# Optimization experiments

Measured on AMD Instinct MI355X. Metric: run time of the kernel, lower is better.

Reference implementation:

```python
import jax, jax.numpy as jnp
import numpy as np

PI = float(np.pi)


def _layernorm(x, g, b, eps=1e-5):
    mu = jnp.mean(x, axis=-1, keepdims=True)
    var = jnp.var(x, axis=-1, keepdims=True)
    return (x - mu) * jax.lax.rsqrt(var + eps) * g + b


def setup_inputs() -> dict:
    key = jax.random.key(0)
    B, L, D, P = 4, 2048, 256, 32
    ks = jax.random.split(key, 16)

    def lin_w(k, fi, fo):
        return (jax.random.normal(k, (fi, fo), dtype=jnp.float32) / np.sqrt(fi)).astype(jnp.float32)

    inp = {
        'x': jax.random.normal(ks[0], (B, L, D), dtype=jnp.float32),
        'pos_phases': jax.random.normal(ks[1], (L, P), dtype=jnp.float32) * PI,
        'w_mem1v': lin_w(ks[2], D, P), 'b_mem1v': jnp.zeros((P,), jnp.float32),
        'w_mem1o': lin_w(ks[3], P, D), 'b_mem1o': jnp.zeros((D,), jnp.float32),
        'w_off': lin_w(ks[4], D + P, P), 'b_off': jnp.zeros((P,), jnp.float32),
        'w_key': lin_w(ks[5], D, P), 'b_key': jnp.zeros((P,), jnp.float32),
        'w_val': lin_w(ks[6], D, D), 'b_val': jnp.zeros((D,), jnp.float32),
        'w_sk1': lin_w(ks[7], 2 * D, D), 'b_sk1': jnp.zeros((D,), jnp.float32),
        'w_sk2': lin_w(ks[8], D, P), 'b_sk2': jnp.zeros((P,), jnp.float32),
        'w_gate': lin_w(ks[9], D, 1), 'b_gate': jnp.zeros((1,), jnp.float32),
        'ln_g': jnp.ones((D,), jnp.float32), 'ln_b': jnp.zeros((D,), jnp.float32),
        'w_out': lin_w(ks[10], D, D), 'b_out': jnp.zeros((D,), jnp.float32),
    }
    return inp


def reference(x, pos_phases, w_mem1v, b_mem1v, w_mem1o, b_mem1o, w_off, b_off,
              w_key, b_key, w_val, b_val, w_sk1, b_sk1, w_sk2, b_sk2,
              w_gate, b_gate, ln_g, ln_b, w_out, b_out):
    B, L, D = x.shape
    P = pos_phases.shape[-1]

    pos_cos = jnp.cos(pos_phases)  # [L,P]
    pos_sin = jnp.sin(pos_phases)

    # Memory 1: flat [B,L,P] phasor cumulative memory
    v1 = x @ w_mem1v + b_mem1v                       # [B,L,P]
    mem1_cos = jnp.cumsum(pos_cos[None] * v1, axis=1)
    mem1_sin = jnp.cumsum(pos_sin[None] * v1, axis=1)

    offset_input = jnp.concatenate([x, jnp.broadcast_to(pos_phases[None], (B, L, P))], axis=-1)
    offset = jnp.tanh(offset_input @ w_off + b_off) * PI
    oc, os = jnp.cos(offset), jnp.sin(offset)
    query_cos = pos_cos[None] * oc - pos_sin[None] * os
    query_sin = pos_sin[None] * oc + pos_cos[None] * os
    pos_ret = (mem1_cos * query_cos + mem1_sin * query_sin) / np.sqrt(P)
    pos_out = pos_ret @ w_mem1o + b_mem1o            # [B,L,D]

    # Memory 2: full [B,L,P,D] phasor KV cumulative memory
    key_phases = jnp.tanh(x @ w_key + b_key) * PI    # [B,L,P]
    key_cos, key_sin = jnp.cos(key_phases), jnp.sin(key_phases)
    values = x @ w_val + b_val                       # [B,L,D]
    store_gate = jax.nn.sigmoid(x @ w_gate + b_gate) # [B,L,1]

    positions = jnp.arange(1, L + 1, dtype=x.dtype)[None, :, None]
    context_avg = jnp.cumsum(x, axis=1) / positions
    h = jax.nn.gelu(jnp.concatenate([x, context_avg], axis=-1) @ w_sk1 + b_sk1, approximate=False)
    storage_phases = jnp.tanh(h @ w_sk2 + b_sk2) * PI  # [B,L,P]

    gated_v = values * store_gate                    # [B,L,D]
    kv_mem_cos = jnp.cumsum(jnp.cos(storage_phases)[..., None] * gated_v[:, :, None, :], axis=1)  # [B,L,P,D]
    kv_mem_sin = jnp.cumsum(jnp.sin(storage_phases)[..., None] * gated_v[:, :, None, :], axis=1)

    gate_cumsum = jnp.clip(jnp.cumsum(store_gate, axis=1), 1.0, None)  # [B,L,1]
    kv_retrieved = jnp.einsum('blpd,blp->bld', kv_mem_cos, key_cos) + \
                   jnp.einsum('blpd,blp->bld', kv_mem_sin, key_sin)
    kv_retrieved = kv_retrieved / (jnp.sqrt(gate_cumsum) * np.sqrt(P))

    combined = pos_out + kv_retrieved
    return x + _layernorm(combined, ln_g, ln_b) @ w_out + b_out
```

## Files before the change

kernel.cpp:

```cpp
#include <hip/hip_runtime.h>
#include <hip/hip_bf16.h>

constexpr int B_ = 4;
constexpr int L_ = 2048;
constexpr int D_ = 256;
constexpr int P_ = 32;
constexpr int CL = 32;
constexpr int NC = L_ / CL;

#define PI_F 3.14159265358979323846f
#define INV_SQRT_P 0.17677669529663687f

typedef __attribute__((ext_vector_type(8))) short short8_t;
typedef __attribute__((ext_vector_type(4))) float floatx4;

static __device__ inline short f2bf(float f) {
  unsigned int u;
  __builtin_memcpy(&u, &f, 4);
  unsigned int r = (u + 0x7fffu + ((u >> 16) & 1u)) >> 16;
  return (short)r;
}
static __device__ inline float bf2f(short s) {
  unsigned int u = ((unsigned int)(unsigned short)s) << 16;
  float f;
  __builtin_memcpy(&f, &u, 4);
  return f;
}

__global__ void wprep(const float* __restrict__ x, const float* __restrict__ pos,
                      const float* __restrict__ w_val, const float* __restrict__ w_mem1v,
                      const float* __restrict__ w_off, const float* __restrict__ b_off,
                      const float* __restrict__ w_key, const float* __restrict__ w_gate,
                      const float* __restrict__ w_sk1, const float* __restrict__ w_out,
                      const float* __restrict__ w_sk2, const float* __restrict__ w_mem1o,
                      short* __restrict__ WA, short* __restrict__ W1,
                      short* __restrict__ WO, short* __restrict__ W2T,
                      short* __restrict__ W1OT,
                      short* __restrict__ xbf, float* __restrict__ poff,
                      float* __restrict__ ctxsum) {
  __shared__ float2 psum[2][128];
  int blk = blockIdx.x, tid = threadIdx.x;
  if (blk < 384) {
    int idx = blk * 256 + tid;
    int n = idx >> 8, k = idx & 255;
    float v;
    if (n < 256) v = w_val[k * 256 + n];
    else if (n < 288) v = w_mem1v[k * 32 + (n - 256)];
    else if (n < 320) v = w_off[k * 32 + (n - 288)];
    else if (n < 352) v = w_key[k * 32 + (n - 320)];
    else if (n == 352) v = w_gate[k];
    else v = 0.f;
    WA[idx] = f2bf(v);
  } else if (blk < 896) {
    int idx = (blk - 384) * 256 + tid;
    int n = idx >> 9, k = idx & 511;
    W1[idx] = f2bf(w_sk1[k * 256 + n]);
  } else if (blk < 1152) {
    int idx = (blk - 896) * 256 + tid;
    int n = idx >> 8, k = idx & 255;
    WO[idx] = f2bf(w_out[k * 256 + n]);
  } else if (blk < 1184) {
    int idx = (blk - 1152) * 256 + tid;
    int p = idx >> 8, k = idx & 255;
    W2T[idx] = f2bf(w_sk2[k * 32 + p]);
  } else if (blk < 1216) {
    int idx = (blk - 1184) * 256 + tid;
    int d = idx >> 5, p = idx & 31;
    W1OT[idx] = f2bf(w_mem1o[p * 256 + d]);
  } else if (blk < 1472) {
    int idx = (blk - 1216) * 256 + tid;
    int l = idx >> 5, p = idx & 31;
    float a = b_off[p];
#pragma unroll 8
    for (int j = 0; j < 32; ++j) a += pos[l * 32 + j] * w_off[(256 + j) * 32 + p];
    poff[idx] = a;
  } else {
    int c2 = blk - 1472;
    int b = c2 >> 6, ch = c2 & 63;
    int d2 = (tid & 127) * 2, h = tid >> 7;
    int tokb = b * L_ + ch * 32 + h * 16;
    float2 xv[16];
#pragma unroll
    for (int i = 0; i < 16; ++i)
      xv[i] = *(const float2*)&x[(tokb + i) * 256 + d2];
    float2 s = {0.f, 0.f};
#pragma unroll
    for (int i = 0; i < 16; ++i) { s.x += xv[i].x; s.y += xv[i].y; }
#pragma unroll
    for (int i = 0; i < 16; ++i) {
      short2 o;
      o.x = f2bf(xv[i].x);
      o.y = f2bf(xv[i].y);
      *(short2*)&xbf[(tokb + i) * 256 + d2] = o;
    }
    psum[h][tid & 127] = s;
    __syncthreads();
    if (h == 0) {
      float2 o = psum[1][tid & 127];
      float2 tot = {s.x + o.x, s.y + o.y};
      *(float2*)&ctxsum[c2 * 256 + d2] = tot;
    }
  }
}

__global__ __launch_bounds__(768, 6) void gemmA3(const short* __restrict__ xbf,
                                                 const short* __restrict__ WA,
                                                 const float* __restrict__ pos,
                                                 const float* __restrict__ poff,
                                                 const float* __restrict__ b_mem1v,
                                                 const float* __restrict__ b_key,
                                                 const float* __restrict__ b_gate,
                                                 const float* __restrict__ b_val,
                                                 float* __restrict__ m1cT,
                                                 float* __restrict__ m1sT,
                                                 float* __restrict__ qc,
                                                 float* __restrict__ qs,
                                                 short* __restrict__ K2bf,
                                                 short* __restrict__ gvT,
                                                 float* __restrict__ sg) {
  __shared__ float YL[16][132];
  __shared__ float gsh[16];
  int tid = threadIdx.x;
  int lane = tid & 63, w = tid >> 6;
  int ml = lane & 15, quad = lane >> 4, kq = quad * 8;
  int bc = blockIdx.x;
  int bc32 = bc >> 1, half = bc & 1;
  int tok0 = bc * 16;
  floatx4 acc[2] = {};
  const short* A0p = &xbf[(tok0 + ml) * 256 + kq];
  const short* Bp = &WA[(w * 32 + ml) * 256 + kq];
#pragma unroll
  for (int ks = 0; ks < 8; ++ks) {
    short8_t a0 = *(const short8_t*)(A0p + ks * 32);
#pragma unroll
    for (int nt = 0; nt < 2; ++nt) {
      short8_t b = *(const short8_t*)(Bp + nt * 16 * 256 + ks * 32);
      acc[nt] = __builtin_amdgcn_mfma_f32_16x16x32_bf16(a0, b, acc[nt], 0, 0, 0);
    }
  }
  if (w >= 8) {
#pragma unroll
    for (int nt = 0; nt < 2; ++nt) {
      int col = (w - 8) * 32 + nt * 16 + ml;
#pragma unroll
      for (int r = 0; r < 4; ++r)
        YL[quad * 4 + r][col] = acc[nt][r];
    }
  }
  __syncthreads();
  if (tid < 512) {
    int t = tid >> 5, p = tid & 31;
    int tok = tok0 + t, l = tok & (L_ - 1);
    int b = tok >> 11;
    float v1 = YL[t][p] + b_mem1v[p];
    float ph = pos[l * 32 + p];
    float pc = cosf(ph), ps = sinf(ph);
    int idxT = (b * 32 + p) * L_ + l;
    m1cT[idxT] = pc * v1;
    m1sT[idxT] = ps * v1;
    float off = tanhf(YL[t][32 + p] + poff[l * 32 + p]) * PI_F;
    float oc = cosf(off), os = sinf(off);
    int gidx = tok * 32 + p;
    qc[gidx] = pc * oc - ps * os;
    qs[gidx] = ps * oc + pc * os;
    float kp = tanhf(YL[t][64 + p] + b_key[p]) * PI_F;
    K2bf[tok * 64 + p] = f2bf(cosf(kp));
    K2bf[tok * 64 + 32 + p] = f2bf(sinf(kp));
    if (p == 0) {
      float g = 1.f / (1.f + expf(-(YL[t][96] + b_gate[0])));
      sg[tok] = g;
      gsh[t] = g;
    }
  }
  __syncthreads();
  if (w < 8) {
#pragma unroll
    for (int nt = 0; nt < 2; ++nt) {
      int d = w * 32 + nt * 16 + ml;
      float bv = b_val[d];
      int t0 = quad * 4;
      short4 o;
      o.x = f2bf((acc[nt][0] + bv) * gsh[t0 + 0]);
      o.y = f2bf((acc[nt][1] + bv) * gsh[t0 + 1]);
      o.z = f2bf((acc[nt][2] + bv) * gsh[t0 + 2]);
      o.w = f2bf((acc[nt][3] + bv) * gsh[t0 + 3]);
      *(short4*)&gvT[(bc32 * 256 + d) * 32 + half * 16 + t0] = o;
    }
  }
}

__global__ void scan_all(float* __restrict__ m1cT, float* __restrict__ m1sT,
                         float* __restrict__ sg, float* __restrict__ ctxsum) {
  int blk = blockIdx.x;
  int tid = threadIdx.x;
  if (blk >= 260) {
    int b = blk - 260;
    int base = b * 64 * 256 + tid;
    float v[64];
#pragma unroll
    for (int c = 0; c < 64; ++c) v[c] = ctxsum[base + c * 256];
    float run = 0.f;
#pragma unroll
    for (int c = 0; c < 64; ++c) {
      ctxsum[base + c * 256] = run;
      run += v[c];
    }
    return;
  }
  __shared__ float wsum[4];
  int lane = tid & 63, w = tid >> 6;
  float* arr;
  int base;
  if (blk < 256) {
    arr = (blk < 128) ? m1cT : m1sT;
    base = (blk & 127) * L_;
  } else {
    arr = sg;
    base = (blk - 256) * L_;
  }
  int sbase = base + w * 512;
  float v[8];
#pragma unroll
  for (int i = 0; i < 8; ++i) v[i] = arr[sbase + i * 64 + lane];
  float carry = 0.f;
#pragma unroll
  for (int i = 0; i < 8; ++i) {
    float vv = v[i];
#pragma unroll
    for (int off = 1; off < 64; off <<= 1) {
      float n = __shfl_up(vv, off, 64);
      if (lane >= off) vv += n;
    }
    vv += carry;
    v[i] = vv;
    carry = __shfl(vv, 63, 64);
  }
  if (lane == 0) wsum[w] = carry;
  __syncthreads();
  float off = 0.f;
  for (int ww = 0; ww < w; ++ww) off += wsum[ww];
#pragma unroll
  for (int i = 0; i < 8; ++i) arr[sbase + i * 64 + lane] = v[i] + off;
}

union __align__(16) CDMem {
  short As[32][520];
  struct { short HS[32][280]; short SPL[64][40]; } h;
};
__global__ __launch_bounds__(1024, 4) void gemmCD(const short* __restrict__ xbf,
                                                  const float* __restrict__ x,
                                                  const float* __restrict__ ctxsum,
                                                  const short* __restrict__ W1,
                                                  const float* __restrict__ b_sk1,
                                                  const short* __restrict__ W2T,
                                                  const float* __restrict__ b_sk2,
                                                  const short* __restrict__ gvT,
                                                  short* __restrict__ SPbf,
                                                  short* __restrict__ UT) {
  __shared__ CDMem sm;
  __shared__ float stmp[4][256];
  int tid = threadIdx.x;
  int bc = blockIdx.x;
  int tok0 = bc * 32;
  int bI = bc >> 6, ch = bc & 63;
  int lane = tid & 63, w = tid >> 6;
  int ml = lane & 15, quad = lane >> 4, kq = quad * 8;
  {
    int row = tid >> 5, c8 = tid & 31;
    *(short8_t*)&sm.As[row][c8 * 8] =
        *(const short8_t*)&xbf[(tok0 + row) * 256 + c8 * 8];
  }
  {
    int d = tid & 255, qh = tid >> 8;
    float cp = ctxsum[(bI * 64 + ch) * 256 + d];
    float xv[8];
    int xb = (tok0 + qh * 8) * 256 + d;
#pragma unroll
    for (int i = 0; i < 8; ++i) xv[i] = x[xb + i * 256];
    float p = 0.f;
#pragma unroll
    for (int i = 0; i < 8; ++i) p += xv[i];
    stmp[qh][d] = p;
    __syncthreads();
    float run = cp;
    for (int j = 0; j < qh; ++j) run += stmp[j][d];
    int l0 = ch * 32 + qh * 8;
#pragma unroll
    for (int i = 0; i < 8; ++i) {
      run += xv[i];
      sm.As[qh * 8 + i][256 + d] = f2bf(run / (float)(l0 + i + 1));
    }
  }
  __syncthreads();
  int n0w = w * 16;
  floatx4 acc[2] = {};
#pragma unroll
  for (int kt = 0; kt < 16; ++kt) {
    short8_t a0 = *(short8_t*)&sm.As[ml][kt * 32 + kq];
    short8_t a1 = *(short8_t*)&sm.As[16 + ml][kt * 32 + kq];
    short8_t b0 = *(const short8_t*)&W1[(n0w + ml) * 512 + kt * 32 + kq];
    acc[0] = __builtin_amdgcn_mfma_f32_16x16x32_bf16(a0, b0, acc[0], 0, 0, 0);
    acc[1] = __builtin_amdgcn_mfma_f32_16x16x32_bf16(a1, b0, acc[1], 0, 0, 0);
  }
  short hv[2][4];
  {
    float bv = b_sk1[n0w + ml];
#pragma unroll
    for (int mt = 0; mt < 2; ++mt)
#pragma unroll
      for (int r = 0; r < 4; ++r) {
        float v = acc[mt][r] + bv;
        float g = 0.5f * v * (1.f + erff(v * 0.70710678118654752f));
        hv[mt][r] = f2bf(g);
      }
  }
  __syncthreads();
#pragma unroll
  for (int mt = 0; mt < 2; ++mt)
#pragma unroll
    for (int r = 0; r < 4; ++r)
      sm.h.HS[mt * 16 + quad * 4 + r][n0w + ml] = hv[mt][r];
  __syncthreads();
  if (w < 4) {
    int th = w & 1, ph = w >> 1;
    floatx4 pacc = {};
#pragma unroll
    for (int s = 0; s < 8; ++s) {
      short8_t a = *(short8_t*)&sm.h.HS[th * 16 + ml][s * 32 + kq];
      short8_t b0 = *(const short8_t*)&W2T[(ph * 16 + ml) * 256 + s * 32 + kq];
      pacc = __builtin_amdgcn_mfma_f32_16x16x32_bf16(a, b0, pacc, 0, 0, 0);
    }
    int p = ph * 16 + ml;
    float bs = b_sk2[p];
#pragma unroll
    for (int r = 0; r < 4; ++r) {
      int tl = th * 16 + quad * 4 + r;
      int tok = tok0 + tl;
      float sp = tanhf(pacc[r] + bs) * PI_F;
      short c = f2bf(cosf(sp)), s2 = f2bf(sinf(sp));
      sm.h.SPL[p][tl] = c;
      sm.h.SPL[32 + p][tl] = s2;
      SPbf[tok * 64 + p] = c;
      SPbf[tok * 64 + 32 + p] = s2;
    }
  }
  __syncthreads();
  short8_t a[4];
#pragma unroll
  for (int mt = 0; mt < 4; ++mt) a[mt] = *(short8_t*)&sm.h.SPL[mt * 16 + ml][kq];
  floatx4 acc3[4] = {};
  {
    int d = w * 16 + ml;
    short8_t b = *(const short8_t*)&gvT[(bc * 256 + d) * 32 + kq];
#pragma unroll
    for (int mt = 0; mt < 4; ++mt)
      acc3[mt] = __builtin_amdgcn_mfma_f32_16x16x32_bf16(a[mt], b, acc3[mt], 0, 0, 0);
  }
#pragma unroll
  for (int mt = 0; mt < 4; ++mt) {
    int d = w * 16 + ml;
    short4 o;
    o.x = f2bf(acc3[mt][0]);
    o.y = f2bf(acc3[mt][1]);
    o.z = f2bf(acc3[mt][2]);
    o.w = f2bf(acc3[mt][3]);
    *(short4*)&UT[(bc * 256 + d) * 64 + mt * 16 + quad * 4] = o;
  }
}

__global__ void kernelE(short* __restrict__ UT) {
  int t = blockIdx.x * 256 + threadIdx.x;
  int pi = t >> 2, j = t & 3;
  int q = pi & 63;
  int d = (pi >> 6) & 255;
  int b = pi >> 14;
  const int cs = 256 * 64;
  int base = ((b * NC) * 256 + d) * 64 + q + j * 16 * cs;
  short v[16];
#pragma unroll
  for (int c = 0; c < 16; ++c) v[c] = UT[base + c * cs];
  float tot = 0.f;
#pragma unroll
  for (int c = 0; c < 16; ++c) tot += bf2f(v[c]);
  int lane = threadIdx.x & 63;
  int gb = lane & ~3;
  float t0 = __shfl(tot, gb + 0, 64);
  float t1 = __shfl(tot, gb + 1, 64);
  float t2 = __shfl(tot, gb + 2, 64);
  float run = (j > 0 ? t0 : 0.f) + (j > 1 ? t1 : 0.f) + (j > 2 ? t2 : 0.f);
#pragma unroll
  for (int c = 0; c < 16; ++c) {
    UT[base + c * cs] = f2bf(run);
    run += bf2f(v[c]);
  }
}

struct __align__(16) FGMem {
  short SL[32][40];
  short PR[32][40];
  float CMB[32][260];
  short CBN[32][280];
  float LG[256], LB[256];
  float scl[32], mu_s[32], rs_s[32];
};
__global__ __launch_bounds__(1024, 4) void fgOut(const short* __restrict__ UT,
                                                 const short* __restrict__ SPbf,
                                                 const short* __restrict__ K2bf,
                                                 const short* __restrict__ gvT,
                                                 const float* __restrict__ sgc,
                                                 const float* __restrict__ m1cT,
                                                 const float* __restrict__ m1sT,
                                                 const float* __restrict__ qc,
                                                 const float* __restrict__ qs,
                                                 const short* __restrict__ W1OT,
                                                 const float* __restrict__ b_mem1o,
                                                 const float* __restrict__ ln_g,
                                                 const float* __restrict__ ln_b,
                                                 const short* __restrict__ WO,
                                                 const float* __restrict__ b_out,
                                                 const float* __restrict__ x,
                                                 float* __restrict__ out) {
  __shared__ FGMem sm;
  int tid5 = threadIdx.x;
  int bc = blockIdx.x;
  int lbase = bc * CL;
  int bb = bc >> 6, lloc = (bc & 63) * 32;
  int lane = tid5 & 63, w = tid5 >> 6;
  int ml = lane & 15, quad = lane >> 4, kq = quad * 8;
  int d0 = w * 16;
  if (tid5 < 32) sm.scl[tid5] = rsqrtf(fmaxf(sgc[lbase + tid5], 1.f)) * INV_SQRT_P;
  if (tid5 >= 256 && tid5 < 512) {
    int d = tid5 - 256;
    sm.LG[d] = ln_g[d];
    sm.LB[d] = ln_b[d];
  }
  short8_t ka0 = *(const short8_t*)&K2bf[(lbase + ml) * 64 + kq];
  short8_t ka1 = *(const short8_t*)&K2bf[(lbase + 16 + ml) * 64 + kq];
  short8_t kb0 = *(const short8_t*)&K2bf[(lbase + ml) * 64 + 32 + kq];
  short8_t kb1 = *(const short8_t*)&K2bf[(lbase + 16 + ml) * 64 + 32 + kq];
  if (w == 0) {
    floatx4 sacc[2][2] = {};
#pragma unroll
    for (int ks2 = 0; ks2 < 2; ++ks2) {
      short8_t a0 = (ks2 == 0) ? ka0 : kb0;
      short8_t a1 = (ks2 == 0) ? ka1 : kb1;
      short8_t b0 = *(const short8_t*)&SPbf[(lbase + ml) * 64 + ks2 * 32 + kq];
      short8_t b1 = *(const short8_t*)&SPbf[(lbase + 16 + ml) * 64 + ks2 * 32 + kq];
      sacc[0][0] = __builtin_amdgcn_mfma_f32_16x16x32_bf16(a0, b0, sacc[0][0], 0, 0, 0);
      sacc[0][1] = __builtin_amdgcn_mfma_f32_16x16x32_bf16(a0, b1, sacc[0][1], 0, 0, 0);
      sacc[1][0] = __builtin_amdgcn_mfma_f32_16x16x32_bf16(a1, b0, sacc[1][0], 0, 0, 0);
      sacc[1][1] = __builtin_amdgcn_mfma_f32_16x16x32_bf16(a1, b1, sacc[1][1], 0, 0, 0);
    }
#pragma unroll
    for (int mt = 0; mt < 2; ++mt)
#pragma unroll
      for (int nt = 0; nt < 2; ++nt)
#pragma unroll
        for (int r = 0; r < 4; ++r) {
          int trow = mt * 16 + quad * 4 + r;
          int scol = nt * 16 + ml;
          float v = (scol <= trow) ? sacc[mt][nt][r] : 0.f;
          sm.SL[trow][scol] = f2bf(v);
        }
  } else {
    int t7 = tid5 - 64;
    for (int i = t7; i < 1024; i += 960) {
      int pp = i >> 5, t = i & 31;
      int gT = (bb * 32 + pp) * L_ + lloc + t;
      int g = (lbase + t) * 32 + pp;
      sm.PR[t][pp] = f2bf((m1cT[gT] * qc[g] + m1sT[gT] * qs[g]) * INV_SQRT_P);
    }
  }
  __syncthreads();
  floatx4 acc[2] = {};
  {
    short8_t b0 = *(const short8_t*)&UT[(bc * 256 + d0 + ml) * 64 + kq];
    short8_t b1 = *(const short8_t*)&UT[(bc * 256 + d0 + ml) * 64 + 32 + kq];
    acc[0] = __builtin_amdgcn_mfma_f32_16x16x32_bf16(ka0, b0, acc[0], 0, 0, 0);
    acc[1] = __builtin_amdgcn_mfma_f32_16x16x32_bf16(ka1, b0, acc[1], 0, 0, 0);
    acc[0] = __builtin_amdgcn_mfma_f32_16x16x32_bf16(kb0, b1, acc[0], 0, 0, 0);
    acc[1] = __builtin_amdgcn_mfma_f32_16x16x32_bf16(kb1, b1, acc[1], 0, 0, 0);
  }
  {
    short8_t a0 = *(short8_t*)&sm.SL[ml][kq];
    short8_t a1 = *(short8_t*)&sm.SL[16 + ml][kq];
    short8_t b = *(const short8_t*)&gvT[(bc * 256 + d0 + ml) * 32 + kq];
    acc[0] = __builtin_amdgcn_mfma_f32_16x16x32_bf16(a0, b, acc[0], 0, 0, 0);
    acc[1] = __builtin_amdgcn_mfma_f32_16x16x32_bf16(a1, b, acc[1], 0, 0, 0);
  }
  floatx4 macc[2] = {};
  {
    short8_t a0 = *(short8_t*)&sm.PR[ml][kq];
    short8_t a1 = *(short8_t*)&sm.PR[16 + ml][kq];
    short8_t b = *(const short8_t*)&W1OT[(d0 + ml) * 32 + kq];
    macc[0] = __builtin_amdgcn_mfma_f32_16x16x32_bf16(a0, b, macc[0], 0, 0, 0);
    macc[1] = __builtin_amdgcn_mfma_f32_16x16x32_bf16(a1, b, macc[1], 0, 0, 0);
  }
  {
    int d = d0 + ml;
    float bm = b_mem1o[d];
#pragma unroll
    for (int mt = 0; mt < 2; ++mt)
#pragma unroll
      for (int r = 0; r < 4; ++r) {
        int t = mt * 16 + quad * 4 + r;
        sm.CMB[t][d] = acc[mt][r] * sm.scl[t] + macc[mt][r] + bm;
      }
  }
  __syncthreads();
  {
    int t = tid5 >> 5, g = tid5 & 31;
    float s = 0.f, s2 = 0.f;
#pragma unroll
    for (int j = 0; j < 8; ++j) {
      float v = sm.CMB[t][g + j * 32];
      s += v;
      s2 += v * v;
    }
#pragma unroll
    for (int m = 1; m < 32; m <<= 1) {
      s += __shfl_xor(s, m, 64);
      s2 += __shfl_xor(s2, m, 64);
    }
    if (g == 0) {
      float mu = s / (float)D_;
      float var = s2 / (float)D_ - mu * mu;
      sm.mu_s[t] = mu;
      sm.rs_s[t] = rsqrtf(var + 1e-5f);
    }
  }
  __syncthreads();
#pragma unroll
  for (int it = 0; it < 8; ++it) {
    int i = it * 1024 + tid5;
    int t = i >> 8, d = i & 255;
    sm.CBN[t][d] = f2bf((sm.CMB[t][d] - sm.mu_s[t]) * sm.rs_s[t] * sm.LG[d] + sm.LB[d]);
  }
  __syncthreads();
  floatx4 acc2[2] = {};
#pragma unroll
  for (int kt = 0; kt < 8; ++kt) {
    short8_t a0 = *(short8_t*)&sm.CBN[ml][kt * 32 + kq];
    short8_t a1 = *(short8_t*)&sm.CBN[16 + ml][kt * 32 + kq];
    short8_t b = *(const short8_t*)&WO[(d0 + ml) * 256 + kt * 32 + kq];
    acc2[0] = __builtin_amdgcn_mfma_f32_16x16x32_bf16(a0, b, acc2[0], 0, 0, 0);
    acc2[1] = __builtin_amdgcn_mfma_f32_16x16x32_bf16(a1, b, acc2[1], 0, 0, 0);
  }
  {
    int n = d0 + ml;
    float bv = b_out[n];
#pragma unroll
    for (int mt = 0; mt < 2; ++mt)
#pragma unroll
      for (int r = 0; r < 4; ++r) {
        int tok = lbase + mt * 16 + quad * 4 + r;
        out[tok * 256 + n] = x[tok * 256 + n] + acc2[mt][r] + bv;
      }
  }
}

extern "C" void kernel_launch(void* const* d_in, const int* in_sizes, int n_in,
                              void* d_out, int out_size, void* d_ws, size_t ws_size,
                              hipStream_t stream) {
  const float* x = (const float*)d_in[0];
  const float* pos = (const float*)d_in[1];
  const float* w_mem1v = (const float*)d_in[2];
  const float* b_mem1v = (const float*)d_in[3];
  const float* w_mem1o = (const float*)d_in[4];
  const float* b_mem1o = (const float*)d_in[5];
  const float* w_off = (const float*)d_in[6];
  const float* b_off = (const float*)d_in[7];
  const float* w_key = (const float*)d_in[8];
  const float* b_key = (const float*)d_in[9];
  const float* w_val = (const float*)d_in[10];
  const float* b_val = (const float*)d_in[11];
  const float* w_sk1 = (const float*)d_in[12];
  const float* b_sk1 = (const float*)d_in[13];
  const float* w_sk2 = (const float*)d_in[14];
  const float* b_sk2 = (const float*)d_in[15];
  const float* w_gate = (const float*)d_in[16];
  const float* b_gate = (const float*)d_in[17];
  const float* ln_g = (const float*)d_in[18];
  const float* ln_b = (const float*)d_in[19];
  const float* w_out = (const float*)d_in[20];
  const float* b_out = (const float*)d_in[21];
  float* out = (float*)d_out;
  float* ws = (float*)d_ws;

  const int BLP = B_ * L_ * P_;
  const int BLD = B_ * L_ * D_;
  float* m1cT = ws;
  float* m1sT = m1cT + BLP;
  float* qc = m1sT + BLP;
  float* qs = qc + BLP;
  float* sg = qs + BLP;
  float* poff = sg + B_ * L_;
  float* ctxsum = poff + L_ * P_;
  short* UT = (short*)(ctxsum + B_ * 64 * 256);
  short* xbf = UT + (size_t)B_ * NC * 256 * 64;
  short* ctxbf = xbf + BLD;
  short* hs = ctxbf + BLD;
  short* gvT = hs + BLD;
  short* K2bf = gvT + BLD;
  short* SPbf = K2bf + B_ * L_ * 64;
  short* WA = SPbf + B_ * L_ * 64;
  short* W1 = WA + 384 * 256;
  short* WO = W1 + 256 * 512;
  short* W2T = WO + 256 * 256;
  short* W1OT = W2T + 32 * 256;

  wprep<<<1728, 256, 0, stream>>>(x, pos, w_val, w_mem1v, w_off, b_off, w_key, w_gate,
                                  w_sk1, w_out, w_sk2, w_mem1o, WA, W1, WO, W2T, W1OT,
                                  xbf, poff, ctxsum);
  gemmA3<<<512, 768, 0, stream>>>(xbf, WA, pos, poff, b_mem1v, b_key, b_gate, b_val,
                                  m1cT, m1sT, qc, qs, K2bf, gvT, sg);
  scan_all<<<264, 256, 0, stream>>>(m1cT, m1sT, sg, ctxsum);
  gemmCD<<<256, 1024, 0, stream>>>(xbf, x, ctxsum, W1, b_sk1, W2T, b_sk2, gvT, SPbf, UT);
  kernelE<<<1024, 256, 0, stream>>>(UT);
  fgOut<<<256, 1024, 0, stream>>>(UT, SPbf, K2bf, gvT, sg, m1cT, m1sT, qc, qs,
                                  W1OT, b_mem1o, ln_g, ln_b, WO, b_out, x, out);
}
```

Before: 166.1 us.

## Fold scan kernels into neighbors to cut kernel launches

The ctxsum chunk-prefix scan moves into gemmA3 as four extra blocks. The m1/sg scans move after gemmCD and merge with the UT chunk scan into one scanE kernel, since gemmCD does not consume them. This removes one kernel launch and its inter-kernel gap from the pipeline. The risk is that the extra tail blocks in gemmA3 use 768-thread blocks of which only 256 threads do work, and that the ctxsum scan now runs on just four blocks in a looped form.

After: 162.7 us. 2.1% less time.

```diff
diff --git a/kernel.cpp b/kernel.cpp
--- a/kernel.cpp
+++ b/kernel.cpp
@@ -117,13 +117,32 @@
                                                  float* __restrict__ qs,
                                                  short* __restrict__ K2bf,
                                                  short* __restrict__ gvT,
-                                                 float* __restrict__ sg) {
+                                                 float* __restrict__ sg,
+                                                 float* __restrict__ ctxsum) {
   __shared__ float YL[16][132];
   __shared__ float gsh[16];
   int tid = threadIdx.x;
+  int bc = blockIdx.x;
+  if (bc >= 512) {
+    if (tid < 256) {
+      int b = bc - 512;
+      int base = b * 64 * 256 + tid;
+      float run = 0.f;
+      for (int c0 = 0; c0 < 64; c0 += 8) {
+        float v[8];
+#pragma unroll
+        for (int j = 0; j < 8; ++j) v[j] = ctxsum[base + (c0 + j) * 256];
+#pragma unroll
+        for (int j = 0; j < 8; ++j) {
+          ctxsum[base + (c0 + j) * 256] = run;
+          run += v[j];
+        }
+      }
+    }
+    return;
+  }
   int lane = tid & 63, w = tid >> 6;
   int ml = lane & 15, quad = lane >> 4, kq = quad * 8;
-  int bc = blockIdx.x;
   int bc32 = bc >> 1, half = bc & 1;
   int tok0 = bc * 16;
   floatx4 acc[2] = {};
@@ -189,60 +208,6 @@
   }
 }
 
-__global__ void scan_all(float* __restrict__ m1cT, float* __restrict__ m1sT,
-                         float* __restrict__ sg, float* __restrict__ ctxsum) {
-  int blk = blockIdx.x;
-  int tid = threadIdx.x;
-  if (blk >= 260) {
-    int b = blk - 260;
-    int base = b * 64 * 256 + tid;
-    float v[64];
-#pragma unroll
-    for (int c = 0; c < 64; ++c) v[c] = ctxsum[base + c * 256];
-    float run = 0.f;
-#pragma unroll
-    for (int c = 0; c < 64; ++c) {
-      ctxsum[base + c * 256] = run;
-      run += v[c];
-    }
-    return;
-  }
-  __shared__ float wsum[4];
-  int lane = tid & 63, w = tid >> 6;
-  float* arr;
-  int base;
-  if (blk < 256) {
-    arr = (blk < 128) ? m1cT : m1sT;
-    base = (blk & 127) * L_;
-  } else {
-    arr = sg;
-    base = (blk - 256) * L_;
-  }
-  int sbase = base + w * 512;
-  float v[8];
-#pragma unroll
-  for (int i = 0; i < 8; ++i) v[i] = arr[sbase + i * 64 + lane];
-  float carry = 0.f;
-#pragma unroll
-  for (int i = 0; i < 8; ++i) {
-    float vv = v[i];
-#pragma unroll
-    for (int off = 1; off < 64; off <<= 1) {
-      float n = __shfl_up(vv, off, 64);
-      if (lane >= off) vv += n;
-    }
-    vv += carry;
-    v[i] = vv;
-    carry = __shfl(vv, 63, 64);
-  }
-  if (lane == 0) wsum[w] = carry;
-  __syncthreads();
-  float off = 0.f;
-  for (int ww = 0; ww < w; ++ww) off += wsum[ww];
-#pragma unroll
-  for (int i = 0; i < 8; ++i) arr[sbase + i * 64 + lane] = v[i] + off;
-}
-
 union __align__(16) CDMem {
   short As[32][520];
   struct { short HS[32][280]; short SPL[64][40]; } h;
@@ -368,31 +333,71 @@
   }
 }
 
-__global__ void kernelE(short* __restrict__ UT) {
-  int t = blockIdx.x * 256 + threadIdx.x;
-  int pi = t >> 2, j = t & 3;
-  int q = pi & 63;
-  int d = (pi >> 6) & 255;
-  int b = pi >> 14;
-  const int cs = 256 * 64;
-  int base = ((b * NC) * 256 + d) * 64 + q + j * 16 * cs;
-  short v[16];
-#pragma unroll
-  for (int c = 0; c < 16; ++c) v[c] = UT[base + c * cs];
-  float tot = 0.f;
-#pragma unroll
-  for (int c = 0; c < 16; ++c) tot += bf2f(v[c]);
-  int lane = threadIdx.x & 63;
-  int gb = lane & ~3;
-  float t0 = __shfl(tot, gb + 0, 64);
-  float t1 = __shfl(tot, gb + 1, 64);
-  float t2 = __shfl(tot, gb + 2, 64);
-  float run = (j > 0 ? t0 : 0.f) + (j > 1 ? t1 : 0.f) + (j > 2 ? t2 : 0.f);
-#pragma unroll
-  for (int c = 0; c < 16; ++c) {
-    UT[base + c * cs] = f2bf(run);
-    run += bf2f(v[c]);
-  }
+__global__ void scanE(float* __restrict__ m1cT, float* __restrict__ m1sT,
+                      float* __restrict__ sg, short* __restrict__ UT) {
+  int blk = blockIdx.x;
+  int tid = threadIdx.x;
+  if (blk >= 260) {
+    int t = (blk - 260) * 256 + tid;
+    int pi = t >> 2, j = t & 3;
+    int q = pi & 63;
+    int d = (pi >> 6) & 255;
+    int b = pi >> 14;
+    const int cs = 256 * 64;
+    int base = ((b * NC) * 256 + d) * 64 + q + j * 16 * cs;
+    short v[16];
+#pragma unroll
+    for (int c = 0; c < 16; ++c) v[c] = UT[base + c * cs];
+    float tot = 0.f;
+#pragma unroll
+    for (int c = 0; c < 16; ++c) tot += bf2f(v[c]);
+    int lane = tid & 63;
+    int gb = lane & ~3;
+    float t0 = __shfl(tot, gb + 0, 64);
+    float t1 = __shfl(tot, gb + 1, 64);
+    float t2 = __shfl(tot, gb + 2, 64);
+    float run = (j > 0 ? t0 : 0.f) + (j > 1 ? t1 : 0.f) + (j > 2 ? t2 : 0.f);
+#pragma unroll
+    for (int c = 0; c < 16; ++c) {
+      UT[base + c * cs] = f2bf(run);
+      run += bf2f(v[c]);
+    }
+    return;
+  }
+  __shared__ float wsum[4];
+  int lane = tid & 63, w = tid >> 6;
+  float* arr;
+  int base;
+  if (blk < 256) {
+    arr = (blk < 128) ? m1cT : m1sT;
+    base = (blk & 127) * L_;
+  } else {
+    arr = sg;
+    base = (blk - 256) * L_;
+  }
+  int sbase = base + w * 512;
+  float v[8];
+#pragma unroll
+  for (int i = 0; i < 8; ++i) v[i] = arr[sbase + i * 64 + lane];
+  float carry = 0.f;
+#pragma unroll
+  for (int i = 0; i < 8; ++i) {
+    float vv = v[i];
+#pragma unroll
+    for (int off = 1; off < 64; off <<= 1) {
+      float n = __shfl_up(vv, off, 64);
+      if (lane >= off) vv += n;
+    }
+    vv += carry;
+    v[i] = vv;
+    carry = __shfl(vv, 63, 64);
+  }
+  if (lane == 0) wsum[w] = carry;
+  __syncthreads();
+  float off = 0.f;
+  for (int ww = 0; ww < w; ++ww) off += wsum[ww];
+#pragma unroll
+  for (int i = 0; i < 8; ++i) arr[sbase + i * 64 + lane] = v[i] + off;
 }
 
 struct __align__(16) FGMem {
@@ -612,11 +617,10 @@
   wprep<<<1728, 256, 0, stream>>>(x, pos, w_val, w_mem1v, w_off, b_off, w_key, w_gate,
                                   w_sk1, w_out, w_sk2, w_mem1o, WA, W1, WO, W2T, W1OT,
                                   xbf, poff, ctxsum);
-  gemmA3<<<512, 768, 0, stream>>>(xbf, WA, pos, poff, b_mem1v, b_key, b_gate, b_val,
-                                  m1cT, m1sT, qc, qs, K2bf, gvT, sg);
-  scan_all<<<264, 256, 0, stream>>>(m1cT, m1sT, sg, ctxsum);
+  gemmA3<<<516, 768, 0, stream>>>(xbf, WA, pos, poff, b_mem1v, b_key, b_gate, b_val,
+                                  m1cT, m1sT, qc, qs, K2bf, gvT, sg, ctxsum);
   gemmCD<<<256, 1024, 0, stream>>>(xbf, x, ctxsum, W1, b_sk1, W2T, b_sk2, gvT, SPbf, UT);
-  kernelE<<<1024, 256, 0, stream>>>(UT);
+  scanE<<<1284, 256, 0, stream>>>(m1cT, m1sT, sg, UT);
   fgOut<<<256, 1024, 0, stream>>>(UT, SPbf, K2bf, gvT, sg, m1cT, m1sT, qc, qs,
                                   W1OT, b_mem1o, ln_g, ln_b, WO, b_out, x, out);
 }
```
